# Optimization experiments

Measured on AMD Instinct MI355X. Metric: run time of the kernel, lower is better.

## Reference

```python
import jax, jax.numpy as jnp
import numpy as np

EMBED_DIM = 1024
N_HEADS = 16
HEAD_DIM = EMBED_DIM // N_HEADS
B, N = 4, 2048


def setup_inputs() -> dict:
    key = jax.random.key(0)
    k1, k2, k3, k4, k5 = jax.random.split(key, 5)
    x = jax.random.normal(k1, (B, N, EMBED_DIM), dtype=jnp.float32)
    # Per-head kqv Linear weights stacked: torch Linear(embed_dim, 3*head_dim)
    # torch stores weight as [out, in]; we store transposed [in, out] per head.
    scale = 1.0 / np.sqrt(EMBED_DIM)
    W_kqv = jax.random.uniform(k2, (N_HEADS, EMBED_DIM, 3 * HEAD_DIM), dtype=jnp.float32, minval=-scale, maxval=scale)
    b_kqv = jax.random.uniform(k3, (N_HEADS, 3 * HEAD_DIM), dtype=jnp.float32, minval=-scale, maxval=scale)
    W_proj = jax.random.uniform(k4, (EMBED_DIM, EMBED_DIM), dtype=jnp.float32, minval=-scale, maxval=scale)
    b_proj = jax.random.uniform(k5, (EMBED_DIM,), dtype=jnp.float32, minval=-scale, maxval=scale)
    return {"x": x, "W_kqv": W_kqv, "b_kqv": b_kqv, "W_proj": W_proj, "b_proj": b_proj}


def reference(x, W_kqv, b_kqv, W_proj, b_proj):
    Bx, Nx, D = x.shape
    H = W_kqv.shape[0]
    hd = W_kqv.shape[2] // 3
    # All per-head kqv projections at once: [B, H, N, 3*hd]
    kqv = jnp.einsum('bnd,hde->bhne', x, W_kqv) + b_kqv[None, :, None, :]
    # chunk order in source is (k, q, v)
    k, q, v = jnp.split(kqv, 3, axis=-1)
    # scores scaled by sqrt(head_dim) (D1 in attention_scores is head dim)
    scores = jnp.einsum('bhqd,bhkd->bhqk', q, k) / jnp.sqrt(jnp.float32(hd))
    causal = jnp.tril(jnp.ones((Nx, Nx), dtype=bool))  # [N, N]
    scores = jnp.where(causal[None, None, :, :], scores, -jnp.inf)
    attn = jax.nn.softmax(scores, axis=-1)
    sa = jnp.einsum('bhqk,bhkd->bhqd', attn, v)  # [B, H, N, hd]
    # concat heads along feature dim (head order preserved)
    sa = sa.transpose(0, 2, 1, 3).reshape(Bx, Nx, H * hd)
    # output projection: torch Linear with weight [out, in] -> y = sa @ W^T + b;
    # here W_proj is stored as [in, out]
    return sa @ W_proj + b_proj
```

## Files before the change

kernel.cpp:

```cpp
#include <hip/hip_runtime.h>
#include <math.h>

#define EMBED   1024
#define NHEADS  16
#define HD      64
#define BATCH   4
#define SEQ     2048
#define MROWS   (BATCH*SEQ)
#define NKV     8388608ull

typedef short short8 __attribute__((ext_vector_type(8)));
typedef float floatx4 __attribute__((ext_vector_type(4)));

__device__ __forceinline__ unsigned short f2b(float f) {
    union { float f; unsigned u; } v; v.f = f;
    unsigned r = v.u + 0x7FFFu + ((v.u >> 16) & 1u);
    return (unsigned short)(r >> 16);
}
__device__ __forceinline__ unsigned short f2b_fast(float f) {
    union { float f; unsigned u; } v; v.f = f;
    return (unsigned short)((v.u + 0x8000u) >> 16);
}

#define GLDS16(gp, lp) __builtin_amdgcn_global_load_lds( \
    (const __attribute__((address_space(1))) unsigned int*)(gp), \
    (__attribute__((address_space(3))) unsigned int*)(lp), 16, 0, 0)

__global__ __launch_bounds__(256) void convert_x(
    const float* __restrict__ x, unsigned short* __restrict__ x16)
{
    size_t idx = ((size_t)blockIdx.x * 256 + threadIdx.x) * 8;
    float4 a = *(const float4*)(x + idx);
    float4 b = *(const float4*)(x + idx + 4);
    ushort4 u0, u1;
    u0.x = f2b(a.x); u0.y = f2b(a.y); u0.z = f2b(a.z); u0.w = f2b(a.w);
    u1.x = f2b(b.x); u1.y = f2b(b.y); u1.z = f2b(b.z); u1.w = f2b(b.w);
    *(ushort4*)(x16 + idx) = u0;
    *(ushort4*)(x16 + idx + 4) = u1;
}

__global__ __launch_bounds__(256) void prep_wkqv(
    const float* __restrict__ Wk, unsigned short* __restrict__ Wt)
{
    __shared__ float tile[32][33];
    const int h = blockIdx.z;
    const int k0 = blockIdx.x * 32, e0 = blockIdx.y * 32;
    const float* inh = Wk + (size_t)h * 1024 * 192;
    const int tx = threadIdx.x & 31, ty = threadIdx.x >> 5;
    #pragma unroll
    for (int i = 0; i < 4; i++)
        tile[ty + i * 8][tx] = inh[(size_t)(k0 + ty + i * 8) * 192 + e0 + tx];
    __syncthreads();
    #pragma unroll
    for (int i = 0; i < 4; i++) {
        int e = e0 + ty + i * 8;
        int cp = (e >> 6) * 1024 + h * 64 + (e & 63);
        Wt[(size_t)cp * 1024 + k0 + tx] = f2b(tile[tx][ty + i * 8]);
    }
}

__global__ __launch_bounds__(256) void transpose_w(
    const float* __restrict__ in, unsigned short* __restrict__ outp, int R, int C)
{
    __shared__ float tile[32][33];
    const int r0 = blockIdx.x * 32, c0 = blockIdx.y * 32;
    const int tx = threadIdx.x & 31, ty = threadIdx.x >> 5;
    #pragma unroll
    for (int i = 0; i < 4; i++)
        tile[ty + i * 8][tx] = in[(size_t)(r0 + ty + i * 8) * C + c0 + tx];
    __syncthreads();
    #pragma unroll
    for (int i = 0; i < 4; i++)
        outp[(size_t)(c0 + ty + i * 8) * R + r0 + tx] = f2b(tile[tx][ty + i * 8]);
}

__device__ __forceinline__ void mainloop_128x256(
    const unsigned short* __restrict__ Ag,
    const unsigned short* __restrict__ Bg,
    unsigned short* smem,
    int row0, int col0, floatx4 (&acc)[4][4])
{
    const int t = threadIdx.x;
    const int wave = t >> 6, lane = t & 63;
    const int lr = lane & 15, quad = lane >> 4;
    const int wr = wave >> 2, wc = wave & 3;
    const int swz8 = ((lane & 7) ^ ((lane >> 3) & 7)) * 8;
    const int c0 = (quad ^ (lr & 7)) * 8;
    const int c1 = ((4 + quad) ^ (lr & 7)) * 8;

    #pragma unroll
    for (int m = 0; m < 4; m++)
        #pragma unroll
        for (int n = 0; n < 4; n++) acc[m][n] = (floatx4){0.f, 0.f, 0.f, 0.f};

#define STG(G, R0, KC, L) do { \
    _Pragma("unroll") \
    for (int i_ = 0; i_ < 2; i_++) { \
        int rl_ = i_ * 64 + wave * 8 + (lane >> 3); \
        GLDS16((G) + (size_t)((R0) + rl_) * 1024 + (KC) + swz8, \
               (L) + rl_ * 64 + (lane & 7) * 8); \
    } } while (0)

    STG(Ag, row0,       0,  smem);
    STG(Bg, col0,       0,  smem + 8192);
    STG(Bg, col0 + 128, 0,  smem + 16384);
    STG(Bg, col0,       64, smem + 24576 + 8192);
    STG(Bg, col0 + 128, 64, smem + 24576 + 16384);
    asm volatile("s_waitcnt vmcnt(4)" ::: "memory");
    __builtin_amdgcn_s_barrier();

    #pragma unroll 2
    for (int j = 0; j < 16; ++j) {
        unsigned short* Ab = smem + (j & 1) * 24576;
        unsigned short* Bb = Ab + 8192;
        unsigned short* An = smem + ((j + 1) & 1) * 24576;
        const unsigned short* pA = Ab + (wr * 64 + lr) * 64;
        const unsigned short* pB = Bb + (wc * 64 + lr) * 64;

        short8 af0[4], af1[4], b0[4], b1[4];

        #pragma unroll
        for (int m = 0; m < 4; m++) af0[m] = *(const short8*)(pA + m * 1024 + c0);
        #pragma unroll
        for (int n = 0; n < 4; n++) b0[n] = *(const short8*)(pB + n * 1024 + c0);
        #pragma unroll
        for (int n = 0; n < 4; n++) b1[n] = *(const short8*)(pB + n * 1024 + c1);
        if (j < 15) STG(Ag, row0, (j + 1) * 64, An);
        __builtin_amdgcn_s_barrier();
        asm volatile("s_waitcnt lgkmcnt(0)" ::: "memory");
        __builtin_amdgcn_s_setprio(1);
        #pragma unroll
        for (int m = 0; m < 4; m++)
            #pragma unroll
            for (int n = 0; n < 4; n++)
                acc[m][n] = __builtin_amdgcn_mfma_f32_16x16x32_bf16(af0[m], b0[n], acc[m][n], 0, 0, 0);
        __builtin_amdgcn_s_setprio(0);
        __builtin_amdgcn_s_barrier();

        #pragma unroll
        for (int m = 0; m < 4; m++) af1[m] = *(const short8*)(pA + m * 1024 + c1);
        if (j < 14) {
            STG(Bg, col0,       (j + 2) * 64, Bb);
            STG(Bg, col0 + 128, (j + 2) * 64, Bb + 8192);
        }
        __builtin_amdgcn_s_barrier();
        asm volatile("s_waitcnt lgkmcnt(0)" ::: "memory");
        __builtin_amdgcn_s_setprio(1);
        #pragma unroll
        for (int m = 0; m < 4; m++)
            #pragma unroll
            for (int n = 0; n < 4; n++)
                acc[m][n] = __builtin_amdgcn_mfma_f32_16x16x32_bf16(af1[m], b1[n], acc[m][n], 0, 0, 0);
        __builtin_amdgcn_s_setprio(0);
        if (j < 14)       asm volatile("s_waitcnt vmcnt(4)" ::: "memory");
        else if (j == 14) asm volatile("s_waitcnt vmcnt(0)" ::: "memory");
        __builtin_amdgcn_s_barrier();
    }
#undef STG
}

__global__ __launch_bounds__(512, 2) void gemm_kqv(
    const unsigned short* __restrict__ A,
    const unsigned short* __restrict__ Bt,
    const float* __restrict__ bk,
    unsigned short* __restrict__ Kb16,
    unsigned short* __restrict__ Qb16,
    unsigned short* __restrict__ Vt16)
{
    __shared__ unsigned short smem[49152];

    const int mt = blockIdx.x;
    const int ct = blockIdx.y;
    const int row0 = mt * 128, col0 = ct * 256;

    floatx4 acc[4][4];
    mainloop_128x256(A, Bt, smem, row0, col0, acc);

    const int t = threadIdx.x;
    const int wave = t >> 6, lane = t & 63;
    const int lr = lane & 15, quad = lane >> 4;
    const int wr = wave >> 2, wc = wave & 3;

    unsigned short* W = smem + wave * 4096;
    const int sec = ct >> 2;
    const int h = ((ct & 3) << 2) + wc;
    const int bidx = row0 >> 11;
    const int rbase = (row0 & 2047) + wr * 64;

    float bias[4];
    #pragma unroll
    for (int n = 0; n < 4; n++) bias[n] = bk[h * 192 + sec * 64 + n * 16 + lr];

    if (sec < 2) {
        const float scl = (sec == 1) ? (0.125f * 1.44269504089f) : 1.0f;
        #pragma unroll
        for (int m = 0; m < 4; m++)
            #pragma unroll
            for (int n = 0; n < 4; n++) {
                int es = (n * 16 + lr) ^ (quad << 4);
                #pragma unroll
                for (int r = 0; r < 4; r++)
                    W[(m * 16 + quad * 4 + r) * 64 + es] = f2b((acc[m][n][r] + bias[n]) * scl);
            }
        __syncthreads();
        unsigned short* dst = ((sec == 0) ? Kb16 : Qb16)
                              + ((size_t)(bidx * 16 + h) * 2048 + rbase) * 64;
        const int rrow = lane >> 3, chunk = lane & 7;
        #pragma unroll
        for (int p = 0; p < 8; p++) {
            int row = p * 8 + rrow;
            int ch = chunk ^ (((row >> 2) & 3) << 1);
            *(float4*)(dst + (size_t)row * 64 + chunk * 8) =
                *(const float4*)(W + row * 64 + ch * 8);
        }
    } else {
        #pragma unroll
        for (int m = 0; m < 4; m++)
            #pragma unroll
            for (int n = 0; n < 4; n++) {
                int e = n * 16 + lr;
                ushort4 pk;
                pk.x = f2b(acc[m][n][0] + bias[n]);
                pk.y = f2b(acc[m][n][1] + bias[n]);
                pk.z = f2b(acc[m][n][2] + bias[n]);
                pk.w = f2b(acc[m][n][3] + bias[n]);
                int mp = m ^ (lr & 3);
                *(ushort4*)(W + e * 64 + mp * 16 + quad * 4) = pk;
            }
        __syncthreads();
        unsigned short* dstV = Vt16 + (size_t)(bidx * 16 + h) * 64 * 2048 + rbase;
        const int ev = lane >> 3, chunkR = lane & 7;
        #pragma unroll
        for (int p = 0; p < 8; p++) {
            int e = p * 8 + ev;
            int ch = chunkR ^ ((e & 3) << 1);
            *(float4*)(dstV + (size_t)e * 2048 + chunkR * 8) =
                *(const float4*)(W + e * 64 + ch * 8);
        }
    }
}

__global__ __launch_bounds__(256, 2) void attn_mfma(
    const unsigned short* __restrict__ Kb,
    const unsigned short* __restrict__ Qb,
    const unsigned short* __restrict__ Vt,
    unsigned short* __restrict__ sa)
{
    const int bh = blockIdx.x;
    const int bx = blockIdx.y;
    const int b = bh >> 4, h = bh & 15;
    const int wave = threadIdx.x >> 6;
    const int lane = threadIdx.x & 63;
    const int lr = lane & 15, quad = lane >> 4;
    const int qt_[2] = {bx, 15 - bx};

    __shared__ unsigned short Ks[2][64 * 64];
    __shared__ unsigned short Vs[2][64 * 64];
    __shared__ unsigned short Ps[4][2][16 * 72];

    const unsigned short* Kbh = Kb + (size_t)bh * 2048 * 64;
    const unsigned short* Vbh = Vt + (size_t)bh * 64 * 2048;
    const unsigned short* Qbh = Qb + (size_t)bh * 2048 * 64;

    short8 qf[2][2][2];
    #pragma unroll
    for (int tt = 0; tt < 2; tt++)
        #pragma unroll
        for (int s = 0; s < 2; s++) {
            const unsigned short* qp = Qbh +
                (size_t)(qt_[tt] * 128 + wave * 32 + s * 16 + lr) * 64 + quad * 8;
            qf[tt][s][0] = *(const short8*)(qp);
            qf[tt][s][1] = *(const short8*)(qp + 32);
        }

    floatx4 O[2][2][4];
    float ls[2][2][4];
    #pragma unroll
    for (int tt = 0; tt < 2; tt++)
        #pragma unroll
        for (int s = 0; s < 2; s++) {
            #pragma unroll
            for (int d = 0; d < 4; d++) O[tt][s][d] = (floatx4){0.f, 0.f, 0.f, 0.f};
            #pragma unroll
            for (int r = 0; r < 4; r++) ls[tt][s][r] = 0.f;
        }

    const int r_local = lane >> 3, cc = lane & 7;
    const int swz = cc ^ r_local;
    const int whalf = wave >> 1;

#define STAGE_KV(KT, BSEL) do { \
    const int k0_ = (KT) * 64; \
    _Pragma("unroll") \
    for (int j_ = 0; j_ < 2; j_++) { \
        int R_ = wave * 16 + j_ * 8 + r_local; \
        GLDS16(Kbh + (size_t)(k0_ + R_) * 64 + swz * 8, \
               &Ks[BSEL][0] + (wave * 16 + j_ * 8) * 64 + lane * 8); \
        GLDS16(Vbh + (size_t)R_ * 2048 + k0_ + swz * 8, \
               &Vs[BSEL][0] + (wave * 16 + j_ * 8) * 64 + lane * 8); \
    } } while (0)

    const int ktmax = 2 * qt_[1] + 1;

    STAGE_KV(0, 0);
    asm volatile("s_waitcnt vmcnt(0)" ::: "memory");
    __builtin_amdgcn_s_barrier();

    for (int kt = 0; kt <= ktmax; kt++) {
        const int buf = kt & 1;
        const unsigned short* Ksb = &Ks[buf][0];
        const unsigned short* Vsb = &Vs[buf][0];
        const int k0 = kt * 64;

        if (kt < ktmax) {
            if (buf) STAGE_KV(kt + 1, 0);
            else     STAGE_KV(kt + 1, 1);
        }

        #pragma unroll
        for (int tt = 0; tt < 2; tt++) {
            const int qt2 = qt_[tt];
            const int lim = 2 * qt2 + whalf;
            if (kt > lim) continue;

            floatx4 S[2][4];
            #pragma unroll
            for (int s = 0; s < 2; s++)
                #pragma unroll
                for (int a = 0; a < 4; a++) S[s][a] = (floatx4){0.f, 0.f, 0.f, 0.f};
            #pragma unroll
            for (int c = 0; c < 2; c++)
                #pragma unroll
                for (int a = 0; a < 4; a++) {
                    int R = a * 16 + lr;
                    short8 kf = *(const short8*)(Ksb + R * 64 + (((c * 4 + quad) ^ (lr & 7)) * 8));
                    #pragma unroll
                    for (int s = 0; s < 2; s++)
                        S[s][a] = __builtin_amdgcn_mfma_f32_16x16x32_bf16(qf[tt][s][c], kf, S[s][a], 0, 0, 0);
                }

            if (kt == lim) {
                #pragma unroll
                for (int s = 0; s < 2; s++)
                    #pragma unroll
                    for (int a = 0; a < 4; a++) {
                        int col = k0 + a * 16 + lr;
                        #pragma unroll
                        for (int r = 0; r < 4; r++) {
                            int grow = qt2 * 128 + wave * 32 + s * 16 + quad * 4 + r;
                            if (col > grow) S[s][a][r] = -INFINITY;
                        }
                    }
            }

            #pragma unroll
            for (int s = 0; s < 2; s++)
                #pragma unroll
                for (int a = 0; a < 4; a++)
                    #pragma unroll
                    for (int r = 0; r < 4; r++) {
                        float p = __builtin_amdgcn_exp2f(S[s][a][r]);
                        ls[tt][s][r] += p;
                        Ps[wave][s][(quad * 4 + r) * 72 + a * 16 + lr] = f2b_fast(p);
                    }

            short8 pa[2][2];
            #pragma unroll
            for (int s = 0; s < 2; s++)
                #pragma unroll
                for (int c = 0; c < 2; c++)
                    pa[s][c] = *(const short8*)(Ps[wave][s] + lr * 72 + c * 32 + quad * 8);

            #pragma unroll
            for (int c = 0; c < 2; c++)
                #pragma unroll
                for (int d = 0; d < 4; d++) {
                    int R = d * 16 + lr;
                    short8 vf = *(const short8*)(Vsb + R * 64 + (((c * 4 + quad) ^ (lr & 7)) * 8));
                    #pragma unroll
                    for (int s = 0; s < 2; s++)
                        O[tt][s][d] = __builtin_amdgcn_mfma_f32_16x16x32_bf16(pa[s][c], vf, O[tt][s][d], 0, 0, 0);
                }
        }

        asm volatile("s_waitcnt vmcnt(0)" ::: "memory");
        __builtin_amdgcn_s_barrier();
    }
#undef STAGE_KV

    #pragma unroll
    for (int tt = 0; tt < 2; tt++)
        #pragma unroll
        for (int s = 0; s < 2; s++)
            #pragma unroll
            for (int r = 0; r < 4; r++) {
                float sm = ls[tt][s][r];
                sm += __shfl_xor(sm, 1);
                sm += __shfl_xor(sm, 2);
                sm += __shfl_xor(sm, 4);
                sm += __shfl_xor(sm, 8);
                float inv = 1.0f / sm;
                size_t base = ((size_t)(b * 2048 + qt_[tt] * 128 + wave * 32 + s * 16 + quad * 4 + r)) * 1024
                              + h * 64 + lr;
                #pragma unroll
                for (int d = 0; d < 4; d++)
                    sa[base + d * 16] = f2b(O[tt][s][d][r] * inv);
            }
}

__global__ __launch_bounds__(512, 2) void gemm_proj(
    const unsigned short* __restrict__ A,
    const unsigned short* __restrict__ Bt,
    const float* __restrict__ bp,
    float* __restrict__ out)
{
    __shared__ unsigned short smem[49152];

    const int mt = blockIdx.x;
    const int ct = blockIdx.y;
    const int row0 = mt * 128, col0 = ct * 256;

    floatx4 acc[4][4];
    mainloop_128x256(A, Bt, smem, row0, col0, acc);

    const int t = threadIdx.x;
    const int lane = t & 63, wave = t >> 6;
    const int lr = lane & 15, quad = lane >> 4;
    const int wr = wave >> 2, wc = wave & 3;

    float bias[4]; int cols[4];
    #pragma unroll
    for (int n = 0; n < 4; n++) {
        cols[n] = col0 + wc * 64 + n * 16 + lr;
        bias[n] = bp[cols[n]];
    }
    #pragma unroll
    for (int a = 0; a < 4; a++) {
        #pragma unroll
        for (int n = 0; n < 4; n++) {
            #pragma unroll
            for (int r = 0; r < 4; r++) {
                int m = row0 + wr * 64 + a * 16 + quad * 4 + r;
                out[(size_t)m * 1024 + cols[n]] = acc[a][n][r] + bias[n];
            }
        }
    }
}

extern "C" void kernel_launch(void* const* d_in, const int* in_sizes, int n_in,
                              void* d_out, int out_size, void* d_ws, size_t ws_size,
                              hipStream_t stream) {
    const float* x  = (const float*)d_in[0];
    const float* Wk = (const float*)d_in[1];
    const float* bk = (const float*)d_in[2];
    const float* Wp = (const float*)d_in[3];
    const float* bp = (const float*)d_in[4];
    float* out = (float*)d_out;

    unsigned short* Kb16 = (unsigned short*)d_ws;
    unsigned short* Qb16 = Kb16 + NKV;
    unsigned short* Vt16 = Qb16 + NKV;
    unsigned short* sa16 = Vt16 + NKV;
    unsigned short* x16  = sa16 + 8388608ull;
    unsigned short* Wt   = x16  + 8388608ull;
    unsigned short* Wpt  = Wt   + 3145728ull;

    convert_x<<<4096, 256, 0, stream>>>(x, x16);
    prep_wkqv<<<dim3(32, 6, 16), 256, 0, stream>>>(Wk, Wt);
    transpose_w<<<dim3(32, 32, 1), 256, 0, stream>>>(Wp, Wpt, 1024, 1024);
    gemm_kqv<<<dim3(64, 12), 512, 0, stream>>>(x16, Wt, bk, Kb16, Qb16, Vt16);
    attn_mfma<<<dim3(64, 8), 256, 0, stream>>>(Kb16, Qb16, Vt16, sa16);
    gemm_proj<<<dim3(64, 4), 512, 0, stream>>>(sa16, Wpt, bp, out);
}
```

Before: 234.3 us.

## Triple-buffer LDS tiles in shared GEMM mainloop for deeper prefetch

Switches the 128x256 GEMM mainloop from a double-buffered scheme, where A and B tiles were staggered by a half-iteration, to a three-stage rotating buffer for both A and B. Loads are now issued two k-steps ahead and vmcnt waits relaxed to 6, which hides more global-to-LDS latency. LDS per block grows from 96 KB to 144 KB in both gemm_kqv and gemm_proj. This likely stops two blocks from fitting per CU as the launch bounds request, trading occupancy for deeper prefetch. The b1 fragment loads are also moved to just before the second MFMA batch, which lowers register pressure.

```diff
diff --git a/kernel.cpp b/kernel.cpp
--- a/kernel.cpp
+++ b/kernel.cpp
@@ -101,31 +101,34 @@
                (L) + rl_ * 64 + (lane & 7) * 8); \
     } } while (0)
 
-    STG(Ag, row0,       0,  smem);
-    STG(Bg, col0,       0,  smem + 8192);
-    STG(Bg, col0 + 128, 0,  smem + 16384);
-    STG(Bg, col0,       64, smem + 24576 + 8192);
-    STG(Bg, col0 + 128, 64, smem + 24576 + 16384);
-    asm volatile("s_waitcnt vmcnt(4)" ::: "memory");
+    unsigned short* aC  = smem;
+    unsigned short* aN  = smem + 8192;
+    unsigned short* aN2 = smem + 16384;
+    unsigned short* bC  = smem + 24576;
+    unsigned short* bN  = smem + 24576 + 16384;
+    unsigned short* bN2 = smem + 24576 + 32768;
+
+    STG(Ag, row0,       0,  aC);
+    STG(Bg, col0,       0,  bC);
+    STG(Bg, col0 + 128, 0,  bC + 8192);
+    STG(Ag, row0,       64, aN);
+    STG(Bg, col0,       64, bN);
+    STG(Bg, col0 + 128, 64, bN + 8192);
+    asm volatile("s_waitcnt vmcnt(6)" ::: "memory");
     __builtin_amdgcn_s_barrier();
 
     #pragma unroll 2
     for (int j = 0; j < 16; ++j) {
-        unsigned short* Ab = smem + (j & 1) * 24576;
-        unsigned short* Bb = Ab + 8192;
-        unsigned short* An = smem + ((j + 1) & 1) * 24576;
-        const unsigned short* pA = Ab + (wr * 64 + lr) * 64;
-        const unsigned short* pB = Bb + (wc * 64 + lr) * 64;
-
-        short8 af0[4], af1[4], b0[4], b1[4];
+        const unsigned short* pA = aC + (wr * 64 + lr) * 64;
+        const unsigned short* pB = bC + (wc * 64 + lr) * 64;
+
+        short8 af0[4], af1[4], b0f[4], b1f[4];
 
         #pragma unroll
         for (int m = 0; m < 4; m++) af0[m] = *(const short8*)(pA + m * 1024 + c0);
         #pragma unroll
-        for (int n = 0; n < 4; n++) b0[n] = *(const short8*)(pB + n * 1024 + c0);
-        #pragma unroll
-        for (int n = 0; n < 4; n++) b1[n] = *(const short8*)(pB + n * 1024 + c1);
-        if (j < 15) STG(Ag, row0, (j + 1) * 64, An);
+        for (int n = 0; n < 4; n++) b0f[n] = *(const short8*)(pB + n * 1024 + c0);
+        if (j < 14) STG(Ag, row0, (j + 2) * 64, aN2);
         __builtin_amdgcn_s_barrier();
         asm volatile("s_waitcnt lgkmcnt(0)" ::: "memory");
         __builtin_amdgcn_s_setprio(1);
@@ -133,15 +136,17 @@
         for (int m = 0; m < 4; m++)
             #pragma unroll
             for (int n = 0; n < 4; n++)
-                acc[m][n] = __builtin_amdgcn_mfma_f32_16x16x32_bf16(af0[m], b0[n], acc[m][n], 0, 0, 0);
+                acc[m][n] = __builtin_amdgcn_mfma_f32_16x16x32_bf16(af0[m], b0f[n], acc[m][n], 0, 0, 0);
         __builtin_amdgcn_s_setprio(0);
         __builtin_amdgcn_s_barrier();
 
         #pragma unroll
         for (int m = 0; m < 4; m++) af1[m] = *(const short8*)(pA + m * 1024 + c1);
+        #pragma unroll
+        for (int n = 0; n < 4; n++) b1f[n] = *(const short8*)(pB + n * 1024 + c1);
         if (j < 14) {
-            STG(Bg, col0,       (j + 2) * 64, Bb);
-            STG(Bg, col0 + 128, (j + 2) * 64, Bb + 8192);
+            STG(Bg, col0,       (j + 2) * 64, bN2);
+            STG(Bg, col0 + 128, (j + 2) * 64, bN2 + 8192);
         }
         __builtin_amdgcn_s_barrier();
         asm volatile("s_waitcnt lgkmcnt(0)" ::: "memory");
@@ -150,11 +155,15 @@
         for (int m = 0; m < 4; m++)
             #pragma unroll
             for (int n = 0; n < 4; n++)
-                acc[m][n] = __builtin_amdgcn_mfma_f32_16x16x32_bf16(af1[m], b1[n], acc[m][n], 0, 0, 0);
+                acc[m][n] = __builtin_amdgcn_mfma_f32_16x16x32_bf16(af1[m], b1f[n], acc[m][n], 0, 0, 0);
         __builtin_amdgcn_s_setprio(0);
-        if (j < 14)       asm volatile("s_waitcnt vmcnt(4)" ::: "memory");
+        if (j < 14)       asm volatile("s_waitcnt vmcnt(6)" ::: "memory");
         else if (j == 14) asm volatile("s_waitcnt vmcnt(0)" ::: "memory");
         __builtin_amdgcn_s_barrier();
+
+        unsigned short* r_;
+        r_ = aC; aC = aN; aN = aN2; aN2 = r_;
+        r_ = bC; bC = bN; bN = bN2; bN2 = r_;
     }
 #undef STG
 }
@@ -167,7 +176,7 @@
     unsigned short* __restrict__ Qb16,
     unsigned short* __restrict__ Vt16)
 {
-    __shared__ unsigned short smem[49152];
+    __shared__ unsigned short smem[73728];
 
     const int mt = blockIdx.x;
     const int ct = blockIdx.y;
@@ -414,7 +423,7 @@
     const float* __restrict__ bp,
     float* __restrict__ out)
 {
-    __shared__ unsigned short smem[49152];
+    __shared__ unsigned short smem[73728];
 
     const int mt = blockIdx.x;
     const int ct = blockIdx.y;
```

New measurement: 237.9 us. No clear change (+1.5%).

## Triple-buffer GEMM mainloop with two-ahead prefetch and single barrier per k-tile

Applied to the files above, without the earlier changes.

Replaces the double-buffered GEMM mainloop, which split each k-step into two half-steps with four barriers, with a three-stage LDS ring. A and B tiles are prefetched two k-steps ahead, all fragments are loaded at once, and one barrier is used per k-step. This aims to cut synchronisation overhead and hide global-load latency better. Shared memory per block grows from 96KB to 144KB, which likely limits residency to one block per CU and reduces latency hiding across blocks.

```diff
diff --git a/kernel.cpp b/kernel.cpp
--- a/kernel.cpp
+++ b/kernel.cpp
@@ -101,61 +101,66 @@
                (L) + rl_ * 64 + (lane & 7) * 8); \
     } } while (0)
 
-    STG(Ag, row0,       0,  smem);
-    STG(Bg, col0,       0,  smem + 8192);
-    STG(Bg, col0 + 128, 0,  smem + 16384);
-    STG(Bg, col0,       64, smem + 24576 + 8192);
-    STG(Bg, col0 + 128, 64, smem + 24576 + 16384);
-    asm volatile("s_waitcnt vmcnt(4)" ::: "memory");
+    unsigned short* const a0 = smem;
+    unsigned short* const a1 = smem + 8192;
+    unsigned short* const a2 = smem + 16384;
+    unsigned short* const b0 = smem + 24576;
+    unsigned short* const b1 = smem + 24576 + 16384;
+    unsigned short* const b2 = smem + 24576 + 32768;
+
+#define KTILE(J, AR, BR, AT, BT) do { \
+    const unsigned short* pA_ = (AR) + (wr * 64 + lr) * 64; \
+    const unsigned short* pB_ = (BR) + (wc * 64 + lr) * 64; \
+    short8 af0[4], af1[4], b0f[4], b1f[4]; \
+    _Pragma("unroll") \
+    for (int m = 0; m < 4; m++) { \
+        af0[m] = *(const short8*)(pA_ + m * 1024 + c0); \
+        af1[m] = *(const short8*)(pA_ + m * 1024 + c1); \
+    } \
+    _Pragma("unroll") \
+    for (int n = 0; n < 4; n++) { \
+        b0f[n] = *(const short8*)(pB_ + n * 1024 + c0); \
+        b1f[n] = *(const short8*)(pB_ + n * 1024 + c1); \
+    } \
+    if ((J) < 14) { \
+        STG(Ag, row0,       ((J) + 2) * 64, (AT)); \
+        STG(Bg, col0,       ((J) + 2) * 64, (BT)); \
+        STG(Bg, col0 + 128, ((J) + 2) * 64, (BT) + 8192); \
+    } \
+    asm volatile("s_waitcnt lgkmcnt(0)" ::: "memory"); \
+    __builtin_amdgcn_s_setprio(1); \
+    _Pragma("unroll") \
+    for (int m = 0; m < 4; m++) \
+        _Pragma("unroll") \
+        for (int n = 0; n < 4; n++) \
+            acc[m][n] = __builtin_amdgcn_mfma_f32_16x16x32_bf16(af0[m], b0f[n], acc[m][n], 0, 0, 0); \
+    _Pragma("unroll") \
+    for (int m = 0; m < 4; m++) \
+        _Pragma("unroll") \
+        for (int n = 0; n < 4; n++) \
+            acc[m][n] = __builtin_amdgcn_mfma_f32_16x16x32_bf16(af1[m], b1f[n], acc[m][n], 0, 0, 0); \
+    __builtin_amdgcn_s_setprio(0); \
+    if ((J) < 14)       { asm volatile("s_waitcnt vmcnt(6)" ::: "memory"); } \
+    else if ((J) == 14) { asm volatile("s_waitcnt vmcnt(0)" ::: "memory"); } \
+    __builtin_amdgcn_s_barrier(); \
+} while (0)
+
+    STG(Ag, row0,       0,  a0);
+    STG(Bg, col0,       0,  b0);
+    STG(Bg, col0 + 128, 0,  b0 + 8192);
+    STG(Ag, row0,       64, a1);
+    STG(Bg, col0,       64, b1);
+    STG(Bg, col0 + 128, 64, b1 + 8192);
+    asm volatile("s_waitcnt vmcnt(6)" ::: "memory");
     __builtin_amdgcn_s_barrier();
 
-    #pragma unroll 2
-    for (int j = 0; j < 16; ++j) {
-        unsigned short* Ab = smem + (j & 1) * 24576;
-        unsigned short* Bb = Ab + 8192;
-        unsigned short* An = smem + ((j + 1) & 1) * 24576;
-        const unsigned short* pA = Ab + (wr * 64 + lr) * 64;
-        const unsigned short* pB = Bb + (wc * 64 + lr) * 64;
-
-        short8 af0[4], af1[4], b0[4], b1[4];
-
-        #pragma unroll
-        for (int m = 0; m < 4; m++) af0[m] = *(const short8*)(pA + m * 1024 + c0);
-        #pragma unroll
-        for (int n = 0; n < 4; n++) b0[n] = *(const short8*)(pB + n * 1024 + c0);
-        #pragma unroll
-        for (int n = 0; n < 4; n++) b1[n] = *(const short8*)(pB + n * 1024 + c1);
-        if (j < 15) STG(Ag, row0, (j + 1) * 64, An);
-        __builtin_amdgcn_s_barrier();
-        asm volatile("s_waitcnt lgkmcnt(0)" ::: "memory");
-        __builtin_amdgcn_s_setprio(1);
-        #pragma unroll
-        for (int m = 0; m < 4; m++)
-            #pragma unroll
-            for (int n = 0; n < 4; n++)
-                acc[m][n] = __builtin_amdgcn_mfma_f32_16x16x32_bf16(af0[m], b0[n], acc[m][n], 0, 0, 0);
-        __builtin_amdgcn_s_setprio(0);
-        __builtin_amdgcn_s_barrier();
-
-        #pragma unroll
-        for (int m = 0; m < 4; m++) af1[m] = *(const short8*)(pA + m * 1024 + c1);
-        if (j < 14) {
-            STG(Bg, col0,       (j + 2) * 64, Bb);
-            STG(Bg, col0 + 128, (j + 2) * 64, Bb + 8192);
-        }
-        __builtin_amdgcn_s_barrier();
-        asm volatile("s_waitcnt lgkmcnt(0)" ::: "memory");
-        __builtin_amdgcn_s_setprio(1);
-        #pragma unroll
-        for (int m = 0; m < 4; m++)
-            #pragma unroll
-            for (int n = 0; n < 4; n++)
-                acc[m][n] = __builtin_amdgcn_mfma_f32_16x16x32_bf16(af1[m], b1[n], acc[m][n], 0, 0, 0);
-        __builtin_amdgcn_s_setprio(0);
-        if (j < 14)       asm volatile("s_waitcnt vmcnt(4)" ::: "memory");
-        else if (j == 14) asm volatile("s_waitcnt vmcnt(0)" ::: "memory");
-        __builtin_amdgcn_s_barrier();
-    }
+    for (int j0 = 0; j0 < 15; j0 += 3) {
+        KTILE(j0,     a0, b0, a2, b2);
+        KTILE(j0 + 1, a1, b1, a0, b0);
+        KTILE(j0 + 2, a2, b2, a1, b1);
+    }
+    KTILE(15, a0, b0, a2, b2);
+#undef KTILE
 #undef STG
 }
 
@@ -167,7 +172,7 @@
     unsigned short* __restrict__ Qb16,
     unsigned short* __restrict__ Vt16)
 {
-    __shared__ unsigned short smem[49152];
+    __shared__ unsigned short smem[73728];
 
     const int mt = blockIdx.x;
     const int ct = blockIdx.y;
@@ -414,7 +419,7 @@
     const float* __restrict__ bp,
     float* __restrict__ out)
 {
-    __shared__ unsigned short smem[49152];
+    __shared__ unsigned short smem[73728];
 
     const int mt = blockIdx.x;
     const int ct = blockIdx.y;
```

Result: no change. 235.7 us (+0.6%).
